# Kernel tuning notes

Hardware: AMD Instinct MI355X
Metric: run time of the kernel (lower is better)

The kernel has to match this reference:

```python
import jax, jax.numpy as jnp
import numpy as np

BANDWIDTH = 512.0


def _pairwise_lse(A, B, bandwidth):
    """logsumexp over all pairs of exp(-||a-b||^2 / bandwidth).

    Matches torch: vmap over rows b of B computing logsumexp over A,
    then logsumexp over those row results == single logsumexp over the
    full [Na, Nb] matrix of -sq_dist/bandwidth.
    """
    # squared distances via ||a||^2 + ||b||^2 - 2 a.b  (GEMM-dominated)
    a2 = jnp.sum(A * A, axis=-1)  # [Na]
    b2 = jnp.sum(B * B, axis=-1)  # [Nb]
    d2 = a2[:, None] + b2[None, :] - 2.0 * (A @ B.T)  # [Na, Nb]
    return jax.nn.logsumexp(-d2 / bandwidth)


def setup_inputs() -> dict:
    key = jax.random.key(0)
    kx, ky = jax.random.split(key)
    X = jax.random.normal(kx, (8192, 512), dtype=jnp.float32)
    Y = jax.random.normal(ky, (8192, 512), dtype=jnp.float32)
    return {"X": X, "Y": Y}


def reference(X, Y):
    n = X.shape[0]
    m = Y.shape[0]
    xx = (jnp.exp(_pairwise_lse(X, X, BANDWIDTH)) - n) / (n * (n - 1))
    xy = jnp.exp(_pairwise_lse(X, Y, BANDWIDTH)) / (n * m)
    yy = (jnp.exp(_pairwise_lse(Y, Y, BANDWIDTH)) - m) / (m * (m - 1))
    return xx - 2.0 * xy + yy
```

## Files before the change

kernel.cpp:

```cpp
#include <hip/hip_runtime.h>
#include <math.h>


#define D      512
#define BTM    128
#define BTN    256
#define BK     16
#define KSTEPS (D / BK)

#define AHI 0
#define ALO 256
#define BHI 512
#define BLO 1024

typedef _Float16 half8 __attribute__((ext_vector_type(8)));
typedef __attribute__((ext_vector_type(8)))  short  short8;
typedef __attribute__((ext_vector_type(16))) float  f32x16;

union U4H8 { uint4 u; half8 h; };
union U4S8 { uint4 u; short8 s; };

__device__ __forceinline__ unsigned short bf16_rne(float x) {
    unsigned u = __float_as_uint(x);
    return (unsigned short)((u + 0x7fffu + ((u >> 16) & 1u)) >> 16);
}
__device__ __forceinline__ float bf16_f32(unsigned short b) {
    return __uint_as_float(((unsigned)b) << 16);
}
__device__ __forceinline__ void split8(const float v[8], uint4& hi, uint4& lo) {
    unsigned h[8], l[8];
    #pragma unroll
    for (int j = 0; j < 8; j++) {
        unsigned short bh = bf16_rne(v[j]);
        float r = v[j] - bf16_f32(bh);
        unsigned short bl = bf16_rne(r);
        h[j] = bh; l[j] = bl;
    }
    hi.x = h[0] | (h[1] << 16); hi.y = h[2] | (h[3] << 16);
    hi.z = h[4] | (h[5] << 16); hi.w = h[6] | (h[7] << 16);
    lo.x = l[0] | (l[1] << 16); lo.y = l[2] | (l[3] << 16);
    lo.z = l[4] | (l[5] << 16); lo.w = l[6] | (l[7] << 16);
}

__device__ __forceinline__ void lds16(const uint4* g, uint4* l) {
    __builtin_amdgcn_global_load_lds(
        (const __attribute__((address_space(1))) void*)g,
        (__attribute__((address_space(3))) void*)(unsigned int)(uintptr_t)(void*)l,
        16, 0, 0);
}

__global__ void init_kernel(double* accum, unsigned* minkey) {
    if (threadIdx.x < 3) accum[threadIdx.x] = 0.0;
    if (threadIdx.x < 4) minkey[threadIdx.x] = 0xFFFFFFFFu;
}

__global__ __launch_bounds__(256)
void convert_h_kernel(const float* __restrict__ X, const float* __restrict__ Y,
                      uint4* __restrict__ Xh, uint4* __restrict__ Yh, int npts) {
    const float* src = blockIdx.z ? Y : X;
    uint4*       dst = blockIdx.z ? Yh : Xh;
    const int ks = blockIdx.y;
    const int p  = blockIdx.x * 256 + threadIdx.x;
    if (p >= npts) return;
    const float* s = src + (size_t)p * D + ks * BK;
    float v[16];
    *(float4*)&v[0]  = *(const float4*)(s);
    *(float4*)&v[4]  = *(const float4*)(s + 4);
    *(float4*)&v[8]  = *(const float4*)(s + 8);
    *(float4*)&v[12] = *(const float4*)(s + 12);
    U4H8 a, b;
    #pragma unroll
    for (int j = 0; j < 8; j++) { a.h[j] = (_Float16)v[j]; b.h[j] = (_Float16)v[8 + j]; }
    size_t u = (size_t)ks * npts * 2 + (size_t)(p >> 5) * 64 + (p & 31);
    dst[u] = a.u; dst[u + 32] = b.u;
}

__global__ __launch_bounds__(256)
void row_norms_kernel(const float* __restrict__ X, const float* __restrict__ Y,
                      float* __restrict__ X2, float* __restrict__ Y2, int N, int M) {
    const int wave = threadIdx.x >> 6;
    const int lane = threadIdx.x & 63;
    const int row  = blockIdx.x * 4 + wave;
    const float* src; float* dst; int r;
    if (row < N)          { src = X; dst = X2; r = row; }
    else if (row < N + M) { src = Y; dst = Y2; r = row - N; }
    else return;
    const float* p = src + (size_t)r * D;
    float s = 0.f;
    #pragma unroll
    for (int c = 0; c < D; c += 64) {
        float v = p[c + lane];
        s = fmaf(v, v, s);
    }
    #pragma unroll
    for (int off = 32; off > 0; off >>= 1) s += __shfl_down(s, off);
    if (lane == 0) dst[r] = s;
}

__device__ inline unsigned float_key(float f) {
    unsigned u = __float_as_uint(f);
    return (u & 0x80000000u) ? ~u : (u | 0x80000000u);
}
__device__ inline float key_float(unsigned k) {
    return __uint_as_float((k & 0x80000000u) ? (k ^ 0x80000000u) : ~k);
}

__global__ __launch_bounds__(256)
void diag_min_bits_kernel(const float* __restrict__ X, const float* __restrict__ Y,
                          const float* __restrict__ X2, const float* __restrict__ Y2,
                          unsigned* __restrict__ minkey, int ngx) {
    int b = blockIdx.x;
    const float *src, *n2; int zidx;
    if (b < ngx) { src = X; n2 = X2; zidx = 0; }
    else         { src = Y; n2 = Y2; zidx = 2; b -= ngx; }

    const int tid  = threadIdx.x;
    const int wave = tid >> 6, lane = tid & 63;
    const int grp  = b * 4 + wave;
    const int fp   = lane & 31, fh = lane >> 5;
    const int pt   = grp * 32 + fp;
    const float* s = src + (size_t)pt * D + fh * 8;

    f32x16 acc;
    #pragma unroll
    for (int i = 0; i < 16; i++) acc[i] = 0.f;

    for (int ks = 0; ks < KSTEPS; ks++) {
        float v[8];
        *(float4*)&v[0] = *(const float4*)(s + ks * BK);
        *(float4*)&v[4] = *(const float4*)(s + ks * BK + 4);
        U4S8 hi, lo;
        split8(v, hi.u, lo.u);
        short8 ah = hi.s, al = lo.s;
        acc = __builtin_amdgcn_mfma_f32_32x32x16_bf16(ah, ah, acc, 0, 0, 0);
        acc = __builtin_amdgcn_mfma_f32_32x32x16_bf16(ah, al, acc, 0, 0, 0);
        acc = __builtin_amdgcn_mfma_f32_32x32x16_bf16(al, ah, acc, 0, 0, 0);
    }

    float dmin = 1e30f;
    if (fh == ((fp >> 2) & 1)) {
        int r = (fp & 3) + 4 * (fp >> 3);
        float av = acc[r];
        float rn = n2[pt];
        float cn = rn;
        float d2 = rn + cn - 2.0f * av;
        dmin = d2;
    }
    #pragma unroll
    for (int off = 32; off > 0; off >>= 1) dmin = fminf(dmin, __shfl_down(dmin, off));
    __shared__ float wm[4];
    __shared__ int   wz[4];
    if (lane == 0) { wm[wave] = dmin; wz[wave] = zidx; }
    __syncthreads();
    if (tid == 0)
        atomicMin(&minkey[wz[0]],
                  float_key(fminf(fminf(wm[0], wm[1]), fminf(wm[2], wm[3]))));
}

__global__ __launch_bounds__(256, 2)
void pair_exp_sum_kernel(const uint4* __restrict__ Xh, const uint4* __restrict__ Yh,
                         const float* __restrict__ X2, const float* __restrict__ Y2,
                         double* __restrict__ accum, float* __restrict__ bmin,
                         int N, int M) {
    const int z = blockIdx.z;
    const uint4 *Ah, *Bh; const float *An, *Bn; bool sym; int na, nb;
    if (z == 0)      { Ah = Xh; Bh = Xh; An = X2; Bn = X2; sym = true;  na = N; nb = N; }
    else if (z == 1) { Ah = Xh; Bh = Yh; An = X2; Bn = Y2; sym = false; na = N; nb = M; }
    else             { Ah = Yh; Bh = Yh; An = Y2; Bn = Y2; sym = true;  na = M; nb = M; }
    const int bi = blockIdx.x, bj = blockIdx.y;
    if (sym && (2 * bj + 1) < bi) return;

    __shared__ uint4  smem[2][2048];
    __shared__ float  smN[BTM + BTN];
    __shared__ double wsum[4];
    __shared__ float  wmin[4];

    const int tid  = threadIdx.x;
    const int wave = tid >> 6, lane = tid & 63;
    const int wy = wave >> 1, wx = wave & 1;
    const int row0 = bi * BTM, col0 = bj * BTN;

    if (tid < BTM) smN[tid] = An[row0 + tid];
    smN[BTM + tid] = Bn[col0 + tid];

    const int wl = wave * 64 + lane;
    const size_t strideA = (size_t)na * 2;
    const size_t strideB = (size_t)nb * 2;
    const uint4* gB0 = Bh + (size_t)(col0 >> 5) * 64 + wl;
    const uint4* gB1 = gB0 + 256;
    const half8* gA0 = (const half8*)Ah + ((size_t)(row0 >> 5) + 2 * wy) * 64 + lane;
    const half8* gA1 = gA0 + 64;

    f32x16 acc[2][4];
    #pragma unroll
    for (int g = 0; g < 2; g++)
        #pragma unroll
        for (int c = 0; c < 4; c++)
            #pragma unroll
            for (int i = 0; i < 16; i++) acc[g][c][i] = 0.f;

    auto stage4 = [&](int buf, int ks) {
        #pragma unroll
        for (int j = 0; j < 4; j++) {
            lds16(gB0 + (size_t)(ks + j) * strideB, &smem[buf][j * 512 + wl]);
            lds16(gB1 + (size_t)(ks + j) * strideB, &smem[buf][j * 512 + 256 + wl]);
        }
    };
    half8 Af[8][2];
    auto loadA4 = [&](int ks, int s) {
        #pragma unroll
        for (int j = 0; j < 4; j++) {
            Af[s + j][0] = gA0[(size_t)(ks + j) * strideA];
            Af[s + j][1] = gA1[(size_t)(ks + j) * strideA];
        }
    };
    auto computeK = [&](const uint4* base, int slot) {
        const half8* p = (const half8*)base;
        half8 bh[4];
        #pragma unroll
        for (int c = 0; c < 4; c++) bh[c] = p[(4 * wx + c) * 64 + lane];
        #pragma unroll
        for (int g = 0; g < 2; g++)
            #pragma unroll
            for (int c = 0; c < 4; c++)
                acc[g][c] = __builtin_amdgcn_mfma_f32_32x32x16_f16(Af[slot][g], bh[c], acc[g][c], 0, 0, 0);
    };

    stage4(0, 0);
    loadA4(0, 0);

    #pragma unroll
    for (int it = 1; it < KSTEPS / 4; it++) {
        stage4(it & 1, 4 * it);
        loadA4(4 * it, (it & 1) * 4);
        asm volatile("s_waitcnt vmcnt(16)" ::: "memory");
        __builtin_amdgcn_s_barrier();
        __builtin_amdgcn_sched_barrier(0);
        const int pb = (it - 1) & 1, ps = pb * 4;
        computeK(&smem[pb][0],    ps + 0);
        computeK(&smem[pb][512],  ps + 1);
        computeK(&smem[pb][1024], ps + 2);
        computeK(&smem[pb][1536], ps + 3);
        asm volatile("s_waitcnt lgkmcnt(0)" ::: "memory");
        __builtin_amdgcn_s_barrier();
    }
    asm volatile("s_waitcnt vmcnt(0)" ::: "memory");
    __builtin_amdgcn_s_barrier();
    __builtin_amdgcn_sched_barrier(0);
    computeK(&smem[1][0],    4);
    computeK(&smem[1][512],  5);
    computeK(&smem[1][1024], 6);
    computeK(&smem[1][1536], 7);

    float wgt = 1.f;
    if (sym) {
        int cblk = 2 * bj + wx;
        wgt = (cblk > bi) ? 2.f : (cblk == bi ? 1.f : 0.f);
    }

    const int fp = lane & 31, fh = lane >> 5;
    double s = 0.0;
    float dmin = 1e30f;
    if (wgt != 0.f) {
        const float* rowN = &smN[64 * wy];
        const float* colN = &smN[BTM + 128 * wx];
        const float kC = -0.0028177637517362567f;
        #pragma unroll
        for (int g = 0; g < 2; g++)
            #pragma unroll
            for (int c = 0; c < 4; c++) {
                float cn = colN[32 * c + fp];
                float rs = 0.f;
                #pragma unroll
                for (int r = 0; r < 16; r++) {
                    int r32 = (r & 3) + 8 * (r >> 2) + 4 * fh;
                    float d2 = rowN[32 * g + r32] + cn - 2.0f * acc[g][c][r];
                    dmin = fminf(dmin, d2);
                    rs += exp2f(d2 * kC);
                }
                s += (double)rs;
            }
        s *= (double)wgt;
    }

    #pragma unroll
    for (int off = 32; off > 0; off >>= 1) {
        s += __shfl_down(s, off);
        dmin = fminf(dmin, __shfl_down(dmin, off));
    }
    if (lane == 0) { wsum[wave] = s; wmin[wave] = dmin; }
    __syncthreads();
    if (tid == 0) {
        atomicAdd(&accum[z], wsum[0] + wsum[1] + wsum[2] + wsum[3]);
        if (z == 1)
            bmin[bi * gridDim.y + bj] = fminf(fminf(wmin[0], wmin[1]),
                                              fminf(wmin[2], wmin[3]));
    }
}

__global__ __launch_bounds__(256)
void xy_gmin_kernel(const float* __restrict__ bmin, float* __restrict__ gmin, int nblk) {
    float m = 1e30f;
    for (int i = threadIdx.x; i < nblk; i += 256) m = fminf(m, bmin[i]);
    #pragma unroll
    for (int off = 32; off > 0; off >>= 1) m = fminf(m, __shfl_down(m, off));
    __shared__ float wm[4];
    if ((threadIdx.x & 63) == 0) wm[threadIdx.x >> 6] = m;
    __syncthreads();
    if (threadIdx.x == 0) gmin[0] = fminf(fminf(wm[0], wm[1]), fminf(wm[2], wm[3]));
}

__global__ __launch_bounds__(1024)
void refine_min_kernel(const float* __restrict__ A, const float* __restrict__ B,
                       const float* __restrict__ An, const float* __restrict__ Bn,
                       const float* __restrict__ bmin, const float* __restrict__ gmin,
                       unsigned* __restrict__ minkey, int zidx) {
    const int bi = blockIdx.x;
    const int bj = blockIdx.y;
    if (!(bmin[bi * gridDim.y + bj] < gmin[0] + 0.5f)) return;
    const int row0 = bi * BTM, col0 = bj * BTN;

    __shared__ uint4 smem[1536];
    __shared__ float smN[BTM + BTN];
    __shared__ float wmin[16];

    const int tid  = threadIdx.x;
    const int wave = tid >> 6, lane = tid & 63;
    const int gy = wave & 3, cg0 = 2 * (wave >> 2);
    if (tid < BTM) smN[tid] = An[row0 + tid];
    if (tid < BTN) smN[BTM + tid] = Bn[col0 + tid];

    const int fp = lane & 31, fh = lane >> 5;
    const int au = (32 * gy + fp) * 2 + fh;
    int bu[2];
    #pragma unroll
    for (int c = 0; c < 2; c++) bu[c] = (32 * (cg0 + c) + fp) * 2 + fh;

    f32x16 acc[2];
    #pragma unroll
    for (int c = 0; c < 2; c++)
        #pragma unroll
        for (int i = 0; i < 16; i++) acc[c][i] = 0.f;

    for (int ks = 0; ks < KSTEPS; ks++) {
        __syncthreads();
        if (tid < 256) {
            const float* s = A + (size_t)(row0 + (tid >> 1)) * D + ks * BK + (tid & 1) * 8;
            float v[8];
            *(float4*)&v[0] = *(const float4*)s;
            *(float4*)&v[4] = *(const float4*)(s + 4);
            uint4 hi, lo; split8(v, hi, lo);
            smem[AHI + tid] = hi; smem[ALO + tid] = lo;
        } else if (tid < 768) {
            int u = tid - 256;
            const float* s = B + (size_t)(col0 + (u >> 1)) * D + ks * BK + (u & 1) * 8;
            float v[8];
            *(float4*)&v[0] = *(const float4*)s;
            *(float4*)&v[4] = *(const float4*)(s + 4);
            uint4 hi, lo; split8(v, hi, lo);
            smem[BHI + u] = hi; smem[BLO + u] = lo;
        }
        __syncthreads();
        {
            const short8* p = (const short8*)&smem[0];
            short8 ah = p[AHI + au], al = p[ALO + au];
            short8 bh[2], bl[2];
            #pragma unroll
            for (int c = 0; c < 2; c++) { bh[c] = p[BHI + bu[c]]; bl[c] = p[BLO + bu[c]]; }
            #pragma unroll
            for (int c = 0; c < 2; c++)
                acc[c] = __builtin_amdgcn_mfma_f32_32x32x16_bf16(ah, bh[c], acc[c], 0, 0, 0);
            #pragma unroll
            for (int c = 0; c < 2; c++)
                acc[c] = __builtin_amdgcn_mfma_f32_32x32x16_bf16(ah, bl[c], acc[c], 0, 0, 0);
            #pragma unroll
            for (int c = 0; c < 2; c++)
                acc[c] = __builtin_amdgcn_mfma_f32_32x32x16_bf16(al, bh[c], acc[c], 0, 0, 0);
        }
    }

    float dmin = 1e30f;
    const float* rowN = &smN[32 * gy];
    #pragma unroll
    for (int c = 0; c < 2; c++) {
        float cn = smN[BTM + 32 * (cg0 + c) + fp];
        #pragma unroll
        for (int r = 0; r < 16; r++) {
            int r32 = (r & 3) + 8 * (r >> 2) + 4 * fh;
            float d2 = rowN[r32] + cn - 2.0f * acc[c][r];
            dmin = fminf(dmin, d2);
        }
    }

    #pragma unroll
    for (int off = 32; off > 0; off >>= 1) dmin = fminf(dmin, __shfl_down(dmin, off));
    if (lane == 0) wmin[wave] = dmin;
    __syncthreads();
    if (tid == 0) {
        float m = wmin[0];
        #pragma unroll
        for (int w = 1; w < 16; w++) m = fminf(m, wmin[w]);
        atomicMin(&minkey[zidx], float_key(m));
    }
}

__global__ void finalize_kernel(const double* __restrict__ accum,
                                const unsigned* __restrict__ minkey,
                                float* __restrict__ out, int N, int M) {
    if (threadIdx.x == 0 && blockIdx.x == 0) {
        float Sp[3];
        #pragma unroll
        for (int z = 0; z < 3; z++) {
            float m = key_float(minkey[z]) * (-1.0f / 512.0f);
            double Sshift = accum[z] * exp(-(double)m);
            float r = (float)log(Sshift);
            float lse = r + m;
            Sp[z] = (float)exp((double)lse);
        }
        float nf  = (float)N, mf = (float)M;
        float nn1 = (float)((double)N * (double)(N - 1));
        float mm1 = (float)((double)M * (double)(M - 1));
        float nm  = (float)((double)N * (double)M);
        float xx = (Sp[0] - nf) / nn1;
        float xy =  Sp[1]       / nm;
        float yy = (Sp[2] - mf) / mm1;
        out[0] = xx - 2.0f * xy + yy;
    }
}

extern "C" void kernel_launch(void* const* d_in, const int* in_sizes, int n_in,
                              void* d_out, int out_size, void* d_ws, size_t ws_size,
                              hipStream_t stream) {
    const float* X = (const float*)d_in[0];
    const float* Y = (const float*)d_in[1];
    const int N = in_sizes[0] / D;
    const int M = in_sizes[1] / D;
    const int gx = N / BTM, gy = M / BTN;

    double*   accum  = (double*)d_ws;
    unsigned* minkey = (unsigned*)((char*)d_ws + 32);
    float*    gmin   = (float*)((char*)d_ws + 48);
    float*    X2     = (float*)((char*)d_ws + 64);
    float*    Y2     = X2 + N;
    float*    bmin   = Y2 + M;
    size_t off = (64 + (size_t)(N + M) * 4 + (size_t)gx * gy * 4 + 255) & ~(size_t)255;
    size_t asz = (size_t)N * D * 2;
    uint4* Xh = (uint4*)((char*)d_ws + off);
    uint4* Yh = (uint4*)((char*)d_ws + off + asz);

    init_kernel<<<1, 64, 0, stream>>>(accum, minkey);

    row_norms_kernel<<<(N + M + 3) / 4, 256, 0, stream>>>(X, Y, X2, Y2, N, M);
    convert_h_kernel<<<dim3((N + 255) / 256, KSTEPS, 2), 256, 0, stream>>>(X, Y, Xh, Yh, N);

    diag_min_bits_kernel<<<N / 128 + M / 128, 256, 0, stream>>>(X, Y, X2, Y2, minkey, N / 128);

    dim3 grid(gx, gy, 3);
    pair_exp_sum_kernel<<<grid, 256, 0, stream>>>(Xh, Yh, X2, Y2, accum, bmin, N, M);

    xy_gmin_kernel<<<1, 256, 0, stream>>>(bmin, gmin, gx * gy);
    refine_min_kernel<<<dim3(gx, gy), 1024, 0, stream>>>(X, Y, X2, Y2, bmin, gmin,
                                                         minkey, 1);

    finalize_kernel<<<1, 64, 0, stream>>>(accum, minkey, (float*)d_out, N, M);
}
```

Measured before the change: 306.9 us.

## Stage A tiles through LDS with B and raise occupancy to three blocks

The A fragments were loaded straight from global memory into registers (eight slots per wave). They now go through LDS alongside B, using direct global-to-LDS loads in smaller stages of two k-steps. The LDS footprint per block drops from 64KB to 48KB and A registers are freed, so launch bounds are raised to allow three blocks per CU for better latency hiding. The cost is extra LDS reads for A and a shallower prefetch depth per barrier.

```diff
diff --git a/kernel.cpp b/kernel.cpp
--- a/kernel.cpp
+++ b/kernel.cpp
@@ -157,7 +157,7 @@
                   float_key(fminf(fminf(wm[0], wm[1]), fminf(wm[2], wm[3]))));
 }
 
-__global__ __launch_bounds__(256, 2)
+__global__ __launch_bounds__(256, 3)
 void pair_exp_sum_kernel(const uint4* __restrict__ Xh, const uint4* __restrict__ Yh,
                          const float* __restrict__ X2, const float* __restrict__ Y2,
                          double* __restrict__ accum, float* __restrict__ bmin,
@@ -170,7 +170,7 @@
     const int bi = blockIdx.x, bj = blockIdx.y;
     if (sym && (2 * bj + 1) < bi) return;
 
-    __shared__ uint4  smem[2][2048];
+    __shared__ uint4  smem[2][1536];
     __shared__ float  smN[BTM + BTN];
     __shared__ double wsum[4];
     __shared__ float  wmin[4];
@@ -186,10 +186,9 @@
     const int wl = wave * 64 + lane;
     const size_t strideA = (size_t)na * 2;
     const size_t strideB = (size_t)nb * 2;
+    const uint4* gA0 = Ah + (size_t)(row0 >> 5) * 64 + wl;
     const uint4* gB0 = Bh + (size_t)(col0 >> 5) * 64 + wl;
     const uint4* gB1 = gB0 + 256;
-    const half8* gA0 = (const half8*)Ah + ((size_t)(row0 >> 5) + 2 * wy) * 64 + lane;
-    const half8* gA1 = gA0 + 64;
 
     f32x16 acc[2][4];
     #pragma unroll
@@ -199,58 +198,47 @@
             #pragma unroll
             for (int i = 0; i < 16; i++) acc[g][c][i] = 0.f;
 
-    auto stage4 = [&](int buf, int ks) {
-        #pragma unroll
-        for (int j = 0; j < 4; j++) {
-            lds16(gB0 + (size_t)(ks + j) * strideB, &smem[buf][j * 512 + wl]);
-            lds16(gB1 + (size_t)(ks + j) * strideB, &smem[buf][j * 512 + 256 + wl]);
+    auto stage2 = [&](int buf, int ks) {
+        #pragma unroll
+        for (int j = 0; j < 2; j++) {
+            lds16(gA0 + (size_t)(ks + j) * strideA, &smem[buf][j * 768 + wl]);
+            lds16(gB0 + (size_t)(ks + j) * strideB, &smem[buf][j * 768 + 256 + wl]);
+            lds16(gB1 + (size_t)(ks + j) * strideB, &smem[buf][j * 768 + 512 + wl]);
         }
     };
-    half8 Af[8][2];
-    auto loadA4 = [&](int ks, int s) {
-        #pragma unroll
-        for (int j = 0; j < 4; j++) {
-            Af[s + j][0] = gA0[(size_t)(ks + j) * strideA];
-            Af[s + j][1] = gA1[(size_t)(ks + j) * strideA];
-        }
+    auto computeK = [&](const uint4* base) {
+        const half8* p = (const half8*)base;
+        half8 ah[2], bh[4];
+        #pragma unroll
+        for (int g = 0; g < 2; g++) ah[g] = p[(2 * wy + g) * 64 + lane];
+        #pragma unroll
+        for (int c = 0; c < 4; c++) bh[c] = p[256 + (4 * wx + c) * 64 + lane];
+        #pragma unroll
+        for (int g = 0; g < 2; g++)
+            #pragma unroll
+            for (int c = 0; c < 4; c++)
+                acc[g][c] = __builtin_amdgcn_mfma_f32_32x32x16_f16(ah[g], bh[c], acc[g][c], 0, 0, 0);
     };
-    auto computeK = [&](const uint4* base, int slot) {
-        const half8* p = (const half8*)base;
-        half8 bh[4];
-        #pragma unroll
-        for (int c = 0; c < 4; c++) bh[c] = p[(4 * wx + c) * 64 + lane];
-        #pragma unroll
-        for (int g = 0; g < 2; g++)
-            #pragma unroll
-            for (int c = 0; c < 4; c++)
-                acc[g][c] = __builtin_amdgcn_mfma_f32_32x32x16_f16(Af[slot][g], bh[c], acc[g][c], 0, 0, 0);
-    };
-
-    stage4(0, 0);
-    loadA4(0, 0);
-
-    #pragma unroll
-    for (int it = 1; it < KSTEPS / 4; it++) {
-        stage4(it & 1, 4 * it);
-        loadA4(4 * it, (it & 1) * 4);
-        asm volatile("s_waitcnt vmcnt(16)" ::: "memory");
+
+    stage2(0, 0);
+
+    #pragma unroll
+    for (int it = 1; it < KSTEPS / 2; it++) {
+        stage2(it & 1, 2 * it);
+        asm volatile("s_waitcnt vmcnt(6)" ::: "memory");
         __builtin_amdgcn_s_barrier();
         __builtin_amdgcn_sched_barrier(0);
-        const int pb = (it - 1) & 1, ps = pb * 4;
-        computeK(&smem[pb][0],    ps + 0);
-        computeK(&smem[pb][512],  ps + 1);
-        computeK(&smem[pb][1024], ps + 2);
-        computeK(&smem[pb][1536], ps + 3);
+        const int pb = (it - 1) & 1;
+        computeK(&smem[pb][0]);
+        computeK(&smem[pb][768]);
         asm volatile("s_waitcnt lgkmcnt(0)" ::: "memory");
         __builtin_amdgcn_s_barrier();
     }
     asm volatile("s_waitcnt vmcnt(0)" ::: "memory");
     __builtin_amdgcn_s_barrier();
     __builtin_amdgcn_sched_barrier(0);
-    computeK(&smem[1][0],    4);
-    computeK(&smem[1][512],  5);
-    computeK(&smem[1][1024], 6);
-    computeK(&smem[1][1536], 7);
+    computeK(&smem[1][0]);
+    computeK(&smem[1][768]);
 
     float wgt = 1.f;
     if (sym) {
```

Measured after the change: 785.9 us. 2.56x slower.
